# Performance work log

Hardware: AMD Instinct MI355X
Metric: run time of the kernel (lower is better)

Reference implementation:

```python
import jax, jax.numpy as jnp
import numpy as np

N_NODES = 20000
N_EDGES = 160000
N_GRAPHS = 64
IN_DIM = 1304  # 1280 + 24
NEG_SLOPE = 0.2


def gat_conv(x, src, dst, W, a_src, a_dst, b, heads, out_ch):
    """PyG-style GATConv (source_to_target flow, self loops already appended).
    x: [N, in], W: [in, heads*out], a_src/a_dst: [heads, out], b: [heads*out].
    Returns [N, heads*out] (concat=True)."""
    N = x.shape[0]
    h = (x @ W).reshape(N, heads, out_ch)                 # [N, H, C]
    e_src = jnp.sum(h * a_src[None], axis=-1)             # [N, H]
    e_dst = jnp.sum(h * a_dst[None], axis=-1)             # [N, H]
    e = jax.nn.leaky_relu(e_src[src] + e_dst[dst], NEG_SLOPE)  # [E, H]
    # softmax over incoming edges of each destination node
    e_max = jax.ops.segment_max(e, dst, num_segments=N)   # [N, H]
    e_exp = jnp.exp(e - e_max[dst])
    denom = jax.ops.segment_sum(e_exp, dst, num_segments=N)
    alpha = e_exp / (denom[dst] + 1e-16)                  # [E, H]
    msg = h[src] * alpha[:, :, None]                      # [E, H, C]
    out = jax.ops.segment_sum(msg, dst, num_segments=N)   # [N, H, C]
    return out.reshape(N, heads * out_ch) + b


def setup_inputs() -> dict:
    key = jax.random.key(0)
    ks = jax.random.split(key, 20)
    x = jax.random.normal(ks[0], (N_NODES, IN_DIM), dtype=jnp.float32)
    edge_index = jax.random.randint(ks[1], (2, N_EDGES), 0, N_NODES, dtype=jnp.int32)
    phy = jax.random.normal(ks[2], (N_GRAPHS, 188), dtype=jnp.float32)
    batch = jnp.sort(jax.random.randint(ks[3], (N_NODES,), 0, N_GRAPHS, dtype=jnp.int32))

    def glorot(k, shape):
        fan_in, fan_out = shape[0], shape[-1]
        lim = jnp.sqrt(6.0 / (fan_in + fan_out))
        return jax.random.uniform(k, shape, jnp.float32, -lim, lim)

    params = {
        # conv1: GATConv(1304, 256, heads=3)
        "W1": glorot(ks[4], (IN_DIM, 3 * 256)),
        "a_src1": glorot(ks[5], (3, 256)) * 0.1,
        "a_dst1": glorot(ks[6], (3, 256)) * 0.1,
        "b1": jnp.zeros((3 * 256,), jnp.float32),
        # conv2: GATConv(768, 256, heads=1)
        "W2": glorot(ks[7], (3 * 256, 256)),
        "a_src2": glorot(ks[8], (1, 256)) * 0.1,
        "a_dst2": glorot(ks[9], (1, 256)) * 0.1,
        "b2": jnp.zeros((256,), jnp.float32),
        # fc1
        "fc1_w1": glorot(ks[10], (188, 128)), "fc1_b1": jnp.zeros((128,), jnp.float32),
        "fc1_w2": glorot(ks[11], (128, 128)), "fc1_b2": jnp.zeros((128,), jnp.float32),
        # fc2
        "fc2_w1": glorot(ks[12], (256 + 128, 192)), "fc2_b1": jnp.zeros((192,), jnp.float32),
        "fc2_w2": glorot(ks[13], (192, 2)), "fc2_b2": jnp.zeros((2,), jnp.float32),
    }
    return {"x": x, "edge_index": edge_index, "phy": phy, "batch": batch, **params}


def reference(x, edge_index, phy, batch,
              W1, a_src1, a_dst1, b1,
              W2, a_src2, a_dst2, b2,
              fc1_w1, fc1_b1, fc1_w2, fc1_b2,
              fc2_w1, fc2_b1, fc2_w2, fc2_b2):
    N = x.shape[0]
    # add self loops (PyG GATConv default)
    loops = jnp.arange(N, dtype=edge_index.dtype)
    src = jnp.concatenate([edge_index[0], loops])
    dst = jnp.concatenate([edge_index[1], loops])

    h = gat_conv(x, src, dst, W1, a_src1, a_dst1, b1, heads=3, out_ch=256)
    h = jax.nn.relu(h)  # dropout is identity at inference
    h = gat_conv(h, src, dst, W2, a_src2, a_dst2, b2, heads=1, out_ch=256)

    # global mean pool per graph
    sums = jax.ops.segment_sum(h, batch, num_segments=N_GRAPHS)        # [B, 256]
    cnts = jax.ops.segment_sum(jnp.ones((N,), h.dtype), batch, num_segments=N_GRAPHS)
    pooled = sums / jnp.maximum(cnts, 1.0)[:, None]

    mid = jax.nn.relu(phy @ fc1_w1 + fc1_b1)
    mid = jax.nn.relu(mid @ fc1_w2 + fc1_b2)

    z = jnp.concatenate([pooled, mid], axis=1)                          # [B, 384]
    z = jax.nn.relu(z @ fc2_w1 + fc2_b1)
    logits = z @ fc2_w2 + fc2_b2
    return jax.nn.softmax(logits, axis=1)
```

## Files before the change

kernel.cpp:

```cpp
#include <hip/hip_runtime.h>
#include <hip/hip_bf16.h>
#include <math.h>

#define NN    20000
#define MP1   20224
#define NP    20096
#define E0    160000
#define EL    180000
#define NG    64
#define INDIM 1304
#define K1P   1344
#define GNT   21
#define GNX   3
#define GMB   79
#define NWG1  (GMB * GNX)
#define FB    19
#define NEG_SLOPE 0.2f
#define NSB   20
#define PCH   32

#define ZB    80
#define XB    13272
#define WB    4800

typedef __bf16 bf16x8 __attribute__((ext_vector_type(8)));
typedef __bf16 bf16x4 __attribute__((ext_vector_type(4)));
typedef float  f32x4  __attribute__((ext_vector_type(4)));

__device__ __forceinline__ void gload16(const void* g, void* l) {
    __builtin_amdgcn_global_load_lds(
        (const __attribute__((address_space(1))) void*)g,
        (__attribute__((address_space(3))) void*)l, 16, 0, 0);
}

#define BAR()  { __builtin_amdgcn_s_barrier(); asm volatile("" ::: "memory"); }
#define VMW(n) { asm volatile("s_waitcnt vmcnt(" #n ")" ::: "memory"); __builtin_amdgcn_sched_barrier(0); }

__global__ __launch_bounds__(256)
void init_kernel(uint4* __restrict__ zreg, int n16,
                 const float* __restrict__ X, __hip_bfloat16* __restrict__ Xb,
                 const float* __restrict__ W1, const float* __restrict__ W2,
                 __hip_bfloat16* __restrict__ w1t, __hip_bfloat16* __restrict__ w2t) {
    const int b = blockIdx.x, t = threadIdx.x;
    if (b < ZB) {
        int i = b * 256 + t;
        if (i < n16) zreg[i] = (uint4){0u, 0u, 0u, 0u};
        return;
    }
    if (b < ZB + XB) {
        int idx = (b - ZB) * 256 + t;
        const int nb = K1P / 8;
        int row = idx / nb;
        int cb = (idx - row * nb) * 8;
        union { __hip_bfloat16 h[8]; float4 f4; } u;
        if (row < NN && cb + 8 <= INDIM) {
            const float4* p = (const float4*)(X + (size_t)row * INDIM + cb);
            float4 u0 = p[0], u1 = p[1];
            u.h[0] = __float2bfloat16(u0.x); u.h[1] = __float2bfloat16(u0.y);
            u.h[2] = __float2bfloat16(u0.z); u.h[3] = __float2bfloat16(u0.w);
            u.h[4] = __float2bfloat16(u1.x); u.h[5] = __float2bfloat16(u1.y);
            u.h[6] = __float2bfloat16(u1.z); u.h[7] = __float2bfloat16(u1.w);
        } else {
#pragma unroll
            for (int e = 0; e < 8; e++) {
                float f = (row < NN && cb + e < INDIM) ? X[(size_t)row * INDIM + cb + e] : 0.f;
                u.h[e] = __float2bfloat16(f);
            }
        }
        *(float4*)(Xb + (size_t)row * K1P + cb) = u.f4;
        return;
    }
    {
        int idx = (b - ZB - XB) * 256 + t;
        const int n1 = 768 * K1P;
        if (idx < n1) {
            int n = idx / K1P, k = idx - n * K1P;
            float f = (k < INDIM) ? W1[(size_t)k * 768 + n] : 0.f;
            w1t[idx] = __float2bfloat16(f);
        } else {
            int i2 = idx - n1;
            if (i2 < 256 * 768) {
                int n = i2 / 768, k = i2 - n * 768;
                w2t[i2] = __float2bfloat16(W2[(size_t)k * 256 + n]);
            }
        }
    }
}

__device__ __forceinline__ void stA(const __hip_bfloat16* __restrict__ A, int bm, int kt, int mh,
                                    char* abuf, int w, int l) {
#pragma unroll
    for (int u = 0; u < 2; u++) {
        int rl = (w << 3) + (l >> 3);
        int lrow = u * 128 + mh * 64 + rl;
        int skb = ((l & 7) << 4) ^ ((rl & 7) << 4);
        const char* g = (const char*)(A + (size_t)(bm + lrow) * K1P + kt * 64) + skb;
        gload16(g, abuf + (u * 128 + mh * 64) * 128 + (w << 10));
    }
}

__device__ __forceinline__ void stB(const __hip_bfloat16* __restrict__ Bt, int bn, int kt, int nh,
                                    char* bbuf, int w, int l) {
#pragma unroll
    for (int u = 0; u < 2; u++) {
        int c = u * 2 + (w >> 2);
        int row0 = c * 64 + nh * 32;
        int rl = ((w & 3) << 3) + (l >> 3);
        int skb = ((l & 7) << 4) ^ ((rl & 7) << 4);
        const char* g = (const char*)(Bt + (size_t)(bn + row0 + rl) * K1P + kt * 64) + skb;
        gload16(g, bbuf + row0 * 128 + ((w & 3) << 10));
    }
}

__global__ __launch_bounds__(512)
void gemm256(const __hip_bfloat16* __restrict__ A,
             const __hip_bfloat16* __restrict__ Bt,
             __hip_bfloat16* __restrict__ C,
             const float* __restrict__ a_src, const float* __restrict__ a_dst,
             float* __restrict__ esrc, float* __restrict__ edst, int M,
             const int* __restrict__ ei, const int* __restrict__ off,
             int* __restrict__ cur, int* __restrict__ csr) {
    __shared__ char lds[131072];
    const int t = threadIdx.x;

    if (blockIdx.x >= NWG1) {
        for (int e = (blockIdx.x - NWG1) * 512 + t; e < EL; e += FB * 512) {
            int d = (e < E0) ? ei[E0 + e] : (e - E0);
            int s = (e < E0) ? ei[e] : (e - E0);
            int pos = off[d] + atomicAdd(&cur[d], 1);
            csr[pos] = s;
        }
        return;
    }

    const int w = t >> 6, l = t & 63;
    const int wm = w >> 2, wn = w & 3;
    const int fr = l & 15, fq = l >> 4;
    const int amask = (fr & 7) << 4;

    const int nwg = NWG1;
    const int q8 = nwg >> 3, r8 = nwg & 7;
    const int xcd = blockIdx.x & 7, sub = blockIdx.x >> 3;
    const int logical = (xcd < r8 ? xcd * (q8 + 1) : r8 * (q8 + 1) + (xcd - r8) * q8) + sub;
    const int bm = (logical / GNX) * 256;
    const int bn = (logical % GNX) * 256;

    f32x4 acc[8][4];
#pragma unroll
    for (int i = 0; i < 8; i++)
#pragma unroll
        for (int j = 0; j < 4; j++) acc[i][j] = (f32x4){0.f, 0.f, 0.f, 0.f};

    char* A0 = lds;            char* B0 = lds + 32768;
    char* A1 = lds + 65536;    char* B1 = lds + 98304;

    stA(A, bm, 0, 0, A0, w, l);
    stB(Bt, bn, 0, 0, B0, w, l);
    stA(A, bm, 0, 1, A0, w, l);
    stB(Bt, bn, 0, 1, B0, w, l);
    stA(A, bm, 1, 0, A1, w, l);
    stB(Bt, bn, 1, 0, B1, w, l);
    VMW(8);
    BAR();

    for (int kt = 0; kt < GNT; kt++) {
        char* Ab = lds + (kt & 1) * 65536;
        char* Bb = Ab + 32768;
        char* An = lds + ((kt + 1) & 1) * 65536;
        char* Bn = An + 32768;
        bf16x8 a_c[4][2], b_c0[2][2], b_c1[2][2];

#pragma unroll
        for (int im = 0; im < 4; im++)
#pragma unroll
            for (int kk = 0; kk < 2; kk++)
                a_c[im][kk] = *(const bf16x8*)(Ab + (wm * 128 + im * 16 + fr) * 128 + ((kk * 64 + fq * 16) ^ amask));
#pragma unroll
        for (int jn = 0; jn < 2; jn++)
#pragma unroll
            for (int kk = 0; kk < 2; kk++)
                b_c0[jn][kk] = *(const bf16x8*)(Bb + (wn * 64 + jn * 16 + fr) * 128 + ((kk * 64 + fq * 16) ^ amask));
        if (kt + 1 < GNT) stA(A, bm, kt + 1, 1, An, w, l);
        BAR();
        __builtin_amdgcn_s_setprio(1);
#pragma unroll
        for (int im = 0; im < 4; im++)
#pragma unroll
            for (int jn = 0; jn < 2; jn++)
#pragma unroll
                for (int kk = 0; kk < 2; kk++)
                    acc[im][jn] = __builtin_amdgcn_mfma_f32_16x16x32_bf16(a_c[im][kk], b_c0[jn][kk], acc[im][jn], 0, 0, 0);
        __builtin_amdgcn_s_setprio(0);
        if (kt == GNT - 1) { VMW(0); } else { VMW(6); }
        BAR();

#pragma unroll
        for (int jn = 0; jn < 2; jn++)
#pragma unroll
            for (int kk = 0; kk < 2; kk++)
                b_c1[jn][kk] = *(const bf16x8*)(Bb + (wn * 64 + 32 + jn * 16 + fr) * 128 + ((kk * 64 + fq * 16) ^ amask));
        if (kt + 1 < GNT) stB(Bt, bn, kt + 1, 1, Bn, w, l);
        BAR();
        __builtin_amdgcn_s_setprio(1);
#pragma unroll
        for (int im = 0; im < 4; im++)
#pragma unroll
            for (int jn = 0; jn < 2; jn++)
#pragma unroll
                for (int kk = 0; kk < 2; kk++)
                    acc[im][2 + jn] = __builtin_amdgcn_mfma_f32_16x16x32_bf16(a_c[im][kk], b_c1[jn][kk], acc[im][2 + jn], 0, 0, 0);
        __builtin_amdgcn_s_setprio(0);
        if (kt == GNT - 1) { VMW(2); } else { VMW(10); }
        BAR();

#pragma unroll
        for (int im = 0; im < 4; im++)
#pragma unroll
            for (int kk = 0; kk < 2; kk++)
                a_c[im][kk] = *(const bf16x8*)(Ab + (wm * 128 + 64 + im * 16 + fr) * 128 + ((kk * 64 + fq * 16) ^ amask));
        if (kt + 2 < GNT) stA(A, bm, kt + 2, 0, Ab, w, l);
        BAR();
        __builtin_amdgcn_s_setprio(1);
#pragma unroll
        for (int im = 0; im < 4; im++)
#pragma unroll
            for (int jn = 0; jn < 2; jn++)
#pragma unroll
                for (int kk = 0; kk < 2; kk++)
                    acc[4 + im][jn] = __builtin_amdgcn_mfma_f32_16x16x32_bf16(a_c[im][kk], b_c0[jn][kk], acc[4 + im][jn], 0, 0, 0);
        __builtin_amdgcn_s_setprio(0);
        BAR();

        if (kt + 2 < GNT) stB(Bt, bn, kt + 2, 0, Bb, w, l);
        BAR();
        __builtin_amdgcn_s_setprio(1);
#pragma unroll
        for (int im = 0; im < 4; im++)
#pragma unroll
            for (int jn = 0; jn < 2; jn++)
#pragma unroll
                for (int kk = 0; kk < 2; kk++)
                    acc[4 + im][2 + jn] = __builtin_amdgcn_mfma_f32_16x16x32_bf16(a_c[im][kk], b_c1[jn][kk], acc[4 + im][2 + jn], 0, 0, 0);
        __builtin_amdgcn_s_setprio(0);
        if (kt + 2 < GNT) { VMW(8); }
        else if (kt + 2 == GNT) { VMW(4); }
        BAR();
    }

#pragma unroll
    for (int i = 0; i < 8; i++)
#pragma unroll
        for (int j = 0; j < 4; j++)
#pragma unroll
            for (int r = 0; r < 4; r++) {
                int row = bm + wm * 128 + i * 16 + fq * 4 + r;
                int col = bn + wn * 64 + j * 16 + fr;
                if (row < M) C[(size_t)row * 768 + col] = __float2bfloat16(acc[i][j][r]);
            }

    const int head = bn >> 8;
    float asv[4], adv[4];
#pragma unroll
    for (int j = 0; j < 4; j++) {
        asv[j] = a_src[head * 256 + wn * 64 + j * 16 + fr];
        adv[j] = a_dst[head * 256 + wn * 64 + j * 16 + fr];
    }
    __syncthreads();
    float* eb = (float*)lds;
#pragma unroll
    for (int i = 0; i < 8; i++) {
#pragma unroll
        for (int r = 0; r < 4; r++) {
            float ps = 0.f, pd = 0.f;
#pragma unroll
            for (int j = 0; j < 4; j++) { ps += acc[i][j][r] * asv[j]; pd += acc[i][j][r] * adv[j]; }
#pragma unroll
            for (int o = 8; o >= 1; o >>= 1) { ps += __shfl_xor(ps, o, 64); pd += __shfl_xor(pd, o, 64); }
            if (fr == 0) {
                int rowl = wm * 128 + i * 16 + fq * 4 + r;
                eb[(rowl * 4 + wn) * 2 + 0] = ps;
                eb[(rowl * 4 + wn) * 2 + 1] = pd;
            }
        }
    }
    __syncthreads();
    if (t < 256) {
        int row = bm + t;
        if (row < M) {
            float s = eb[t * 8 + 0] + eb[t * 8 + 2] + eb[t * 8 + 4] + eb[t * 8 + 6];
            float d = eb[t * 8 + 1] + eb[t * 8 + 3] + eb[t * 8 + 5] + eb[t * 8 + 7];
            esrc[row * 3 + head] = s;
            edst[row * 3 + head] = d;
        }
    }
}

__global__ __launch_bounds__(256)
void gemm2_fused(const __hip_bfloat16* __restrict__ A,
                 const __hip_bfloat16* __restrict__ Bt,
                 __hip_bfloat16* __restrict__ C,
                 const float* __restrict__ a_src2, const float* __restrict__ a_dst2,
                 float* __restrict__ esrc, float* __restrict__ edst,
                 int M, int N, int K, int NX) {
    __shared__ __hip_bfloat16 As[2][128 * 32];
    __shared__ __hip_bfloat16 Bs[2][128 * 32];
    const int t = threadIdx.x;
    const int w = t >> 6;
    const int l = t & 63;

    const int nwg = gridDim.x;
    const int q = nwg >> 3, r = nwg & 7;
    const int xcd = blockIdx.x & 7, idx = blockIdx.x >> 3;
    const int logical = (xcd < r ? xcd * (q + 1) : r * (q + 1) + (xcd - r) * q) + idx;
    const int bm = (logical / NX) * 128;
    const int bn = (logical % NX) * 128;

    const int wm = (w >> 1) * 64;
    const int wn = (w & 1) * 64;

    f32x4 acc[4][4];
#pragma unroll
    for (int i = 0; i < 4; i++)
#pragma unroll
        for (int j = 0; j < 4; j++) acc[i][j] = (f32x4){0.f, 0.f, 0.f, 0.f};

    const int sr = t >> 2;
    const int sc = (t & 3) * 8;
    const __hip_bfloat16* a0 = A  + (size_t)(bm + sr)      * K + sc;
    const __hip_bfloat16* a1 = A  + (size_t)(bm + 64 + sr) * K + sc;
    const __hip_bfloat16* b0 = Bt + (size_t)(bn + sr)      * K + sc;
    const __hip_bfloat16* b1 = Bt + (size_t)(bn + 64 + sr) * K + sc;

    const int fr = l & 15;
    const int fq = l >> 4;
    const int NT = K / 32;

    auto stage = [&](int k0, int b) {
        char* asb = (char*)&As[b][0];
        char* bsb = (char*)&Bs[b][0];
        gload16(a0 + k0, asb + w * 1024);
        gload16(a1 + k0, asb + 4096 + w * 1024);
        gload16(b0 + k0, bsb + w * 1024);
        gload16(b1 + k0, bsb + 4096 + w * 1024);
    };

    stage(0, 0);
    __syncthreads();

    for (int kt = 0; kt < NT; kt++) {
        const int cb = kt & 1;
        if (kt + 1 < NT) stage((kt + 1) * 32, cb ^ 1);
        bf16x8 av[4], bv[4];
#pragma unroll
        for (int i = 0; i < 4; i++)
            av[i] = *(const bf16x8*)&As[cb][(wm + i * 16 + fr) * 32 + fq * 8];
#pragma unroll
        for (int j = 0; j < 4; j++)
            bv[j] = *(const bf16x8*)&Bs[cb][(wn + j * 16 + fr) * 32 + fq * 8];
#pragma unroll
        for (int i = 0; i < 4; i++)
#pragma unroll
            for (int j = 0; j < 4; j++)
                acc[i][j] = __builtin_amdgcn_mfma_f32_16x16x32_bf16(av[i], bv[j], acc[i][j], 0, 0, 0);
        __syncthreads();
    }

#pragma unroll
    for (int i = 0; i < 4; i++) {
#pragma unroll
        for (int j = 0; j < 4; j++) {
#pragma unroll
            for (int r2 = 0; r2 < 4; r2++) {
                int row = bm + wm + i * 16 + fq * 4 + r2;
                int col = bn + wn + j * 16 + fr;
                if (row < M) C[(size_t)row * N + col] = __float2bfloat16(acc[i][j][r2]);
            }
        }
    }

    float asv[4], adv[4];
#pragma unroll
    for (int j = 0; j < 4; j++) {
        asv[j] = a_src2[bn + wn + j * 16 + fr];
        adv[j] = a_dst2[bn + wn + j * 16 + fr];
    }
    __syncthreads();
    float* eb = (float*)&As[0][0];
#pragma unroll
    for (int i = 0; i < 4; i++) {
#pragma unroll
        for (int r2 = 0; r2 < 4; r2++) {
            float ps = 0.f, pd = 0.f;
#pragma unroll
            for (int j = 0; j < 4; j++) { ps += acc[i][j][r2] * asv[j]; pd += acc[i][j][r2] * adv[j]; }
#pragma unroll
            for (int o = 8; o >= 1; o >>= 1) { ps += __shfl_xor(ps, o, 64); pd += __shfl_xor(pd, o, 64); }
            if (fr == 0) {
                int rowl = wm + i * 16 + fq * 4 + r2;
                int wnIdx = wn >> 6;
                eb[(rowl * 2 + wnIdx) * 2 + 0] = ps;
                eb[(rowl * 2 + wnIdx) * 2 + 1] = pd;
            }
        }
    }
    __syncthreads();
    if (t < 128) {
        int row = bm + t;
        if (row < M) {
            atomicAdd(&esrc[row], eb[t * 4 + 0] + eb[t * 4 + 2]);
            atomicAdd(&edst[row], eb[t * 4 + 1] + eb[t * 4 + 3]);
        }
    }
}

__global__ void hist_kernel(const int* __restrict__ ei, int* __restrict__ deg) {
    int e = blockIdx.x * 256 + threadIdx.x;
    if (e >= EL) return;
    int d = (e < E0) ? ei[E0 + e] : (e - E0);
    atomicAdd(&deg[d], 1);
}

__global__ __launch_bounds__(1024)
void scan_blk(const int* __restrict__ deg, int* __restrict__ off, int* __restrict__ bsum) {
    __shared__ int wsum[16];
    const int b = blockIdx.x, t = threadIdx.x, lane = t & 63, wv = t >> 6;
    const int i = b * 1024 + t;
    int v = (i < NN) ? deg[i] : 0;
    int x = v;
#pragma unroll
    for (int o = 1; o < 64; o <<= 1) {
        int y = __shfl_up(x, o, 64);
        if (lane >= o) x += y;
    }
    if (lane == 63) wsum[wv] = x;
    __syncthreads();
    if (wv == 0 && lane < 16) {
        int s = wsum[lane];
#pragma unroll
        for (int o = 1; o < 16; o <<= 1) {
            int y = __shfl_up(s, o, 64);
            if (lane >= o) s += y;
        }
        wsum[lane] = s;
    }
    __syncthreads();
    int woff = (wv == 0) ? 0 : wsum[wv - 1];
    if (i < NN) off[i + 1] = woff + x;
    if (t == 1023) bsum[b] = wsum[15];
}

__global__ __launch_bounds__(1024)
void scan_add(int* __restrict__ off, const int* __restrict__ bsum) {
    __shared__ int boffs[NSB];
    const int b = blockIdx.x, t = threadIdx.x;
    if (t < 64) {
        int lane = t;
        int v = (lane < NSB) ? bsum[lane] : 0;
        int x = v;
#pragma unroll
        for (int o = 1; o < 64; o <<= 1) {
            int y = __shfl_up(x, o, 64);
            if (lane >= o) x += y;
        }
        if (lane < NSB) boffs[lane] = x - v;
    }
    __syncthreads();
    const int i = b * 1024 + t;
    if (i < NN) off[i + 1] += boffs[b];
    if (b == 0 && t == 0) off[0] = 0;
}

template<int H, bool RELU, typename OutT>
__global__ __launch_bounds__(256)
void gat_aggregate(const __hip_bfloat16* __restrict__ hfeat,
                   const float* __restrict__ esrc,
                   const float* __restrict__ edst,
                   const int* __restrict__ off, const int* __restrict__ csr,
                   const float* __restrict__ bias,
                   OutT* __restrict__ out, int N) {
    const int wv = threadIdx.x >> 6, lane = threadIdx.x & 63;
    const int pair = blockIdx.x * 4 + wv;
    if (pair >= N * H) return;
    const int n = pair / H;
    const int h = pair - n * H;
    const int beg = off[n];
    const int deg = off[n + 1] - beg;

    const float ed = edst[n * H + h];
    float m = -INFINITY, den = 0.f;
    f32x4 acc = (f32x4){0.f, 0.f, 0.f, 0.f};

    for (int base = 0; base < deg; base += 64) {
        const int i = base + lane;
        int s = 0;
        float lg = -INFINITY;
        if (i < deg) {
            s = csr[beg + i];
            float v = esrc[s * H + h] + ed;
            lg = (v >= 0.f) ? v : NEG_SLOPE * v;
        }
        float cm = lg;
#pragma unroll
        for (int o = 1; o < 64; o <<= 1)
            cm = fmaxf(cm, __shfl_xor(cm, o, 64));
        float nm = fmaxf(m, cm);
        float sc = expf(m - nm);
        den *= sc;
#pragma unroll
        for (int e = 0; e < 4; e++) acc[e] *= sc;
        m = nm;
        float wgt = (i < deg) ? expf(lg - m) : 0.f;
        den += wgt;
        const int cnt = min(64, deg - base);
        for (int j = 0; j < cnt; j++) {
            int sj = __shfl(s, j, 64);
            float wj = __shfl(wgt, j, 64);
            bf16x4 hv = *(const bf16x4*)(hfeat + (size_t)sj * (H * 256) + h * 256 + 4 * lane);
#pragma unroll
            for (int e = 0; e < 4; e++) acc[e] += wj * (float)hv[e];
        }
    }
#pragma unroll
    for (int o = 1; o < 64; o <<= 1) den += __shfl_xor(den, o, 64);

    float inv = 1.f / (den + 1e-16f);
    if constexpr (sizeof(OutT) == 2) {
        bf16x4 r;
#pragma unroll
        for (int e = 0; e < 4; e++) {
            float f = acc[e] * inv + bias[h * 256 + 4 * lane + e];
            if (RELU) f = fmaxf(f, 0.f);
            r[e] = (__bf16)f;
        }
        *(bf16x4*)((__hip_bfloat16*)out + (size_t)n * (H * 256) + h * 256 + 4 * lane) = r;
    } else {
        float4 r;
        float* rp = &r.x;
#pragma unroll
        for (int e = 0; e < 4; e++) {
            float f = acc[e] * inv + bias[h * 256 + 4 * lane + e];
            if (RELU) f = fmaxf(f, 0.f);
            rp[e] = f;
        }
        *(float4*)((float*)out + (size_t)n * (H * 256) + h * 256 + 4 * lane) = r;
    }
}

__device__ __forceinline__ int lower_bound_batch(const int* __restrict__ batch, int key) {
    int lo = 0, hi = NN;
    while (lo < hi) {
        int mid = (lo + hi) >> 1;
        if (batch[mid] < key) lo = mid + 1; else hi = mid;
    }
    return lo;
}

__global__ __launch_bounds__(256)
void pool_partial(const __hip_bfloat16* __restrict__ out2, const int* __restrict__ batch,
                  float* __restrict__ partial, float* __restrict__ cnts) {
    const int g = blockIdx.x, c = blockIdx.y, t = threadIdx.x;
    const int s = lower_bound_batch(batch, g);
    const int e = lower_bound_batch(batch, g + 1);
    float a0 = 0.f, a1 = 0.f, a2 = 0.f, a3 = 0.f;
    int n = s + c;
    for (; n + 3 * PCH < e; n += 4 * PCH) {
        float v0 = __bfloat162float(out2[(size_t)n * 256 + t]);
        float v1 = __bfloat162float(out2[(size_t)(n + PCH) * 256 + t]);
        float v2 = __bfloat162float(out2[(size_t)(n + 2 * PCH) * 256 + t]);
        float v3 = __bfloat162float(out2[(size_t)(n + 3 * PCH) * 256 + t]);
        a0 += v0; a1 += v1; a2 += v2; a3 += v3;
    }
    for (; n < e; n += PCH) a0 += __bfloat162float(out2[(size_t)n * 256 + t]);
    partial[((size_t)g * PCH + c) * 256 + t] = a0 + a1 + a2 + a3;
    if (t == 0 && c == 0) cnts[g] = (float)(e - s);
}

__global__ __launch_bounds__(256)
void head_kernel(const float* __restrict__ partial, const float* __restrict__ cnts,
                 const float* __restrict__ phy,
                 const float* __restrict__ w11, const float* __restrict__ b11,
                 const float* __restrict__ w12, const float* __restrict__ b12,
                 const float* __restrict__ w21, const float* __restrict__ b21,
                 const float* __restrict__ w22, const float* __restrict__ b22,
                 float* __restrict__ out) {
    int g = blockIdx.x, t = threadIdx.x;
    __shared__ float ph[188];
    __shared__ float z[384];
    __shared__ float mid[128];
    __shared__ float t1[192];
    __shared__ float lg[2];
    if (t < 188) ph[t] = phy[g * 188 + t];
    {
        float s = 0.f;
#pragma unroll
        for (int c = 0; c < PCH; c++) s += partial[((size_t)g * PCH + c) * 256 + t];
        z[t] = s / fmaxf(cnts[g], 1.0f);
    }
    __syncthreads();
    if (t < 128) {
        float sm = b11[t];
        for (int k = 0; k < 188; k++) sm += ph[k] * w11[k * 128 + t];
        mid[t] = fmaxf(sm, 0.f);
    }
    __syncthreads();
    if (t < 128) {
        float sm = b12[t];
        for (int k = 0; k < 128; k++) sm += mid[k] * w12[k * 128 + t];
        z[256 + t] = fmaxf(sm, 0.f);
    }
    __syncthreads();
    if (t < 192) {
        float sm = b21[t];
        for (int k = 0; k < 384; k++) sm += z[k] * w21[k * 192 + t];
        t1[t] = fmaxf(sm, 0.f);
    }
    __syncthreads();
    if (t < 2) {
        float sm = b22[t];
        for (int k = 0; k < 192; k++) sm += t1[k] * w22[k * 2 + t];
        lg[t] = sm;
    }
    __syncthreads();
    if (t == 0) {
        float mx = fmaxf(lg[0], lg[1]);
        float e0 = expf(lg[0] - mx), e1 = expf(lg[1] - mx);
        float d = e0 + e1;
        out[g * 2 + 0] = e0 / d;
        out[g * 2 + 1] = e1 / d;
    }
}

extern "C" void kernel_launch(void* const* d_in, const int* in_sizes, int n_in,
                              void* d_out, int out_size, void* d_ws, size_t ws_size,
                              hipStream_t stream) {
    const float* x       = (const float*)d_in[0];
    const int*   ei      = (const int*)  d_in[1];
    const float* phy     = (const float*)d_in[2];
    const int*   batch   = (const int*)  d_in[3];
    const float* W1      = (const float*)d_in[4];
    const float* a_src1  = (const float*)d_in[5];
    const float* a_dst1  = (const float*)d_in[6];
    const float* b1      = (const float*)d_in[7];
    const float* W2      = (const float*)d_in[8];
    const float* a_src2  = (const float*)d_in[9];
    const float* a_dst2  = (const float*)d_in[10];
    const float* b2      = (const float*)d_in[11];
    const float* fc1_w1  = (const float*)d_in[12];
    const float* fc1_b1  = (const float*)d_in[13];
    const float* fc1_w2  = (const float*)d_in[14];
    const float* fc1_b2  = (const float*)d_in[15];
    const float* fc2_w1  = (const float*)d_in[16];
    const float* fc2_b1  = (const float*)d_in[17];
    const float* fc2_w2  = (const float*)d_in[18];
    const float* fc2_b2  = (const float*)d_in[19];
    float* out = (float*)d_out;

    char* base = (char*)d_ws;
    size_t o = 0;
    auto alloc = [&](size_t bytes) { size_t r = o; o += (bytes + 255) & ~255ULL; return r; };

    size_t o_xb   = alloc((size_t)MP1 * K1P * 2);
    size_t o_w1t  = alloc((size_t)768 * K1P * 2);
    size_t o_w2t  = alloc((size_t)256 * 768 * 2);
    size_t o_h1b  = alloc((size_t)NP * 768 * 2);
    size_t o_hob  = alloc((size_t)NP * 768 * 2);
    size_t o_es1  = alloc((size_t)NN * 3 * 4);
    size_t o_ed1  = alloc((size_t)NN * 3 * 4);
    size_t o_es2  = alloc((size_t)NN * 4);
    size_t o_ed2  = alloc((size_t)NN * 4);
    size_t o_deg  = alloc((size_t)(NN + 1) * 4);
    size_t o_cur  = alloc((size_t)NN * 4);
    size_t o_zend = o;
    size_t o_off  = alloc((size_t)(NN + 1) * 4);
    size_t o_csr  = alloc((size_t)EL * 4);
    size_t o_bsum = alloc((size_t)NSB * 4);
    size_t o_part = alloc((size_t)NG * PCH * 256 * 4);
    size_t o_cnts = alloc((size_t)NG * 4);

    __hip_bfloat16* xb   = (__hip_bfloat16*)(base + o_xb);
    __hip_bfloat16* w1t  = (__hip_bfloat16*)(base + o_w1t);
    __hip_bfloat16* w2t  = (__hip_bfloat16*)(base + o_w2t);
    __hip_bfloat16* h1b  = (__hip_bfloat16*)(base + o_h1b);
    __hip_bfloat16* hob  = (__hip_bfloat16*)(base + o_hob);
    __hip_bfloat16* h2b  = (__hip_bfloat16*)(base + o_xb);
    __hip_bfloat16* out2 = (__hip_bfloat16*)(base + o_xb + (size_t)24 * 1024 * 1024);
    float* es1   = (float*)(base + o_es1);
    float* ed1   = (float*)(base + o_ed1);
    float* es2   = (float*)(base + o_es2);
    float* ed2   = (float*)(base + o_ed2);
    int*   deg   = (int*)(base + o_deg);
    int*   cur   = (int*)(base + o_cur);
    int*   offs  = (int*)(base + o_off);
    int*   csr   = (int*)(base + o_csr);
    int*   bsum  = (int*)(base + o_bsum);
    float* part  = (float*)(base + o_part);
    float* cnts  = (float*)(base + o_cnts);

    {
        int n16 = (int)((o_zend - o_es2) / 16);
        init_kernel<<<ZB + XB + WB, 256, 0, stream>>>((uint4*)(base + o_es2), n16,
                                                      x, xb, W1, W2, w1t, w2t);
    }

    hist_kernel<<<(EL + 255) / 256, 256, 0, stream>>>(ei, deg);
    scan_blk<<<NSB, 1024, 0, stream>>>(deg, offs, bsum);
    scan_add<<<NSB, 1024, 0, stream>>>(offs, bsum);

    gemm256<<<NWG1 + FB, 512, 0, stream>>>(xb, w1t, h1b, a_src1, a_dst1, es1, ed1, NN,
                                           ei, offs, cur, csr);
    gat_aggregate<3, true, __hip_bfloat16><<<(NN * 3 + 3) / 4, 256, 0, stream>>>(h1b, es1, ed1, offs, csr, b1, hob, NN);

    gemm2_fused<<<2 * 157, 256, 0, stream>>>(hob, w2t, h2b, a_src2, a_dst2, es2, ed2, NN, 256, 768, 2);
    gat_aggregate<1, false, __hip_bfloat16><<<(NN + 3) / 4, 256, 0, stream>>>(h2b, es2, ed2, offs, csr, b2, out2, NN);

    pool_partial<<<dim3(NG, PCH), 256, 0, stream>>>(out2, batch, part, cnts);
    head_kernel<<<NG, 256, 0, stream>>>(part, cnts, phy,
                                        fc1_w1, fc1_b1, fc1_w2, fc1_b2,
                                        fc2_w1, fc2_b1, fc2_w2, fc2_b2, out);
}
```

Before: 232.9 us.

## Single-buffer gemm256 LDS with in-place half-tile prefetch to raise occupancy

Halves the GEMM's LDS allocation from 128 KiB to 64 KiB. It drops the ping-pong double buffer and instead refills each half of the A/B tile in place as soon as that half has been read into registers. Fewer barriers are issued per k-step, and two workgroups may now fit per CU. The cost is a shallower prefetch distance, so global load latency may be exposed, and the reuse-in-place ordering relies on the vmcnt waits and barriers being exactly right.

```diff
diff --git a/kernel.cpp b/kernel.cpp
--- a/kernel.cpp
+++ b/kernel.cpp
@@ -120,7 +120,7 @@
              float* __restrict__ esrc, float* __restrict__ edst, int M,
              const int* __restrict__ ei, const int* __restrict__ off,
              int* __restrict__ cur, int* __restrict__ csr) {
-    __shared__ char lds[131072];
+    __shared__ char lds[65536];
     const int t = threadIdx.x;
 
     if (blockIdx.x >= NWG1) {
@@ -151,25 +151,20 @@
 #pragma unroll
         for (int j = 0; j < 4; j++) acc[i][j] = (f32x4){0.f, 0.f, 0.f, 0.f};
 
-    char* A0 = lds;            char* B0 = lds + 32768;
-    char* A1 = lds + 65536;    char* B1 = lds + 98304;
-
-    stA(A, bm, 0, 0, A0, w, l);
-    stB(Bt, bn, 0, 0, B0, w, l);
-    stA(A, bm, 0, 1, A0, w, l);
-    stB(Bt, bn, 0, 1, B0, w, l);
-    stA(A, bm, 1, 0, A1, w, l);
-    stB(Bt, bn, 1, 0, B1, w, l);
-    VMW(8);
-    BAR();
+    char* Ab = lds;
+    char* Bb = lds + 32768;
+
+    stA(A, bm, 0, 0, Ab, w, l);
+    stB(Bt, bn, 0, 0, Bb, w, l);
+    stB(Bt, bn, 0, 1, Bb, w, l);
+    stA(A, bm, 0, 1, Ab, w, l);
 
     for (int kt = 0; kt < GNT; kt++) {
-        char* Ab = lds + (kt & 1) * 65536;
-        char* Bb = Ab + 32768;
-        char* An = lds + ((kt + 1) & 1) * 65536;
-        char* Bn = An + 32768;
+        const bool nl = (kt + 1 < GNT);
         bf16x8 a_c[4][2], b_c0[2][2], b_c1[2][2];
 
+        VMW(4);
+        BAR();
 #pragma unroll
         for (int im = 0; im < 4; im++)
 #pragma unroll
@@ -180,8 +175,7 @@
 #pragma unroll
             for (int kk = 0; kk < 2; kk++)
                 b_c0[jn][kk] = *(const bf16x8*)(Bb + (wn * 64 + jn * 16 + fr) * 128 + ((kk * 64 + fq * 16) ^ amask));
-        if (kt + 1 < GNT) stA(A, bm, kt + 1, 1, An, w, l);
-        BAR();
+        if (nl) stA(A, bm, kt + 1, 0, Ab, w, l);
         __builtin_amdgcn_s_setprio(1);
 #pragma unroll
         for (int im = 0; im < 4; im++)
@@ -191,16 +185,15 @@
                 for (int kk = 0; kk < 2; kk++)
                     acc[im][jn] = __builtin_amdgcn_mfma_f32_16x16x32_bf16(a_c[im][kk], b_c0[jn][kk], acc[im][jn], 0, 0, 0);
         __builtin_amdgcn_s_setprio(0);
-        if (kt == GNT - 1) { VMW(0); } else { VMW(6); }
+
+        if (nl) { VMW(4); } else { VMW(2); }
         BAR();
-
 #pragma unroll
         for (int jn = 0; jn < 2; jn++)
 #pragma unroll
             for (int kk = 0; kk < 2; kk++)
                 b_c1[jn][kk] = *(const bf16x8*)(Bb + (wn * 64 + 32 + jn * 16 + fr) * 128 + ((kk * 64 + fq * 16) ^ amask));
-        if (kt + 1 < GNT) stB(Bt, bn, kt + 1, 1, Bn, w, l);
-        BAR();
+        if (nl) stB(Bt, bn, kt + 1, 0, Bb, w, l);
         __builtin_amdgcn_s_setprio(1);
 #pragma unroll
         for (int im = 0; im < 4; im++)
@@ -210,16 +203,15 @@
                 for (int kk = 0; kk < 2; kk++)
                     acc[im][2 + jn] = __builtin_amdgcn_mfma_f32_16x16x32_bf16(a_c[im][kk], b_c1[jn][kk], acc[im][2 + jn], 0, 0, 0);
         __builtin_amdgcn_s_setprio(0);
-        if (kt == GNT - 1) { VMW(2); } else { VMW(10); }
+
+        if (nl) { VMW(4); } else { VMW(0); }
         BAR();
-
 #pragma unroll
         for (int im = 0; im < 4; im++)
 #pragma unroll
             for (int kk = 0; kk < 2; kk++)
                 a_c[im][kk] = *(const bf16x8*)(Ab + (wm * 128 + 64 + im * 16 + fr) * 128 + ((kk * 64 + fq * 16) ^ amask));
-        if (kt + 2 < GNT) stA(A, bm, kt + 2, 0, Ab, w, l);
-        BAR();
+        if (nl) stB(Bt, bn, kt + 1, 1, Bb, w, l);
         __builtin_amdgcn_s_setprio(1);
 #pragma unroll
         for (int im = 0; im < 4; im++)
@@ -229,10 +221,8 @@
                 for (int kk = 0; kk < 2; kk++)
                     acc[4 + im][jn] = __builtin_amdgcn_mfma_f32_16x16x32_bf16(a_c[im][kk], b_c0[jn][kk], acc[4 + im][jn], 0, 0, 0);
         __builtin_amdgcn_s_setprio(0);
-        BAR();
-
-        if (kt + 2 < GNT) stB(Bt, bn, kt + 2, 0, Bb, w, l);
-        BAR();
+
+        if (nl) stA(A, bm, kt + 1, 1, Ab, w, l);
         __builtin_amdgcn_s_setprio(1);
 #pragma unroll
         for (int im = 0; im < 4; im++)
@@ -242,9 +232,6 @@
                 for (int kk = 0; kk < 2; kk++)
                     acc[4 + im][2 + jn] = __builtin_amdgcn_mfma_f32_16x16x32_bf16(a_c[im][kk], b_c1[jn][kk], acc[4 + im][2 + jn], 0, 0, 0);
         __builtin_amdgcn_s_setprio(0);
-        if (kt + 2 < GNT) { VMW(8); }
-        else if (kt + 2 == GNT) { VMW(4); }
-        BAR();
     }
 
 #pragma unroll
```

After: 230.3 us, median of 3. About the same (-1.1%).
